# Kernel tuning notes

Measured on AMD Instinct MI355X. Metric: run time of the kernel, lower is better.

## Reference

```python
import jax, jax.numpy as jnp
import numpy as np

ALPHA = 0.9
EPS = 0.01
LAMBDA_PENALTY = 1.0
THRESHOLD = 0.8
COS_EPS = 1e-8
N, F, E = 8192, 256, 262144


def setup_inputs() -> dict:
    key = jax.random.key(0)
    k1, k2, k3, k4, k5 = jax.random.split(key, 5)
    z = jax.random.normal(k1, (N, F), dtype=jnp.float32)
    x_hat = jax.random.normal(k2, (N, F), dtype=jnp.float32)
    edge_index = jax.random.randint(k3, (2, E), 0, N, dtype=jnp.int64)
    f_k2u = jax.random.randint(k4, (N,), 0, 6, dtype=jnp.int64)
    f_u2k = jax.random.randint(k5, (N,), 0, 32, dtype=jnp.int64)
    return {"z": z, "x_hat": x_hat, "edge_index": edge_index,
            "f_k2u": f_k2u, "f_u2k": f_u2k, "epoch": 10}


def _corrcoef_features(z):
    # torch.corrcoef(z.T): correlation between the F feature columns over N nodes
    zm = z - jnp.mean(z, axis=0, keepdims=True)        # [N, F]
    cov = zm.T @ zm                                    # [F, F] (scale cancels in corr)
    std = jnp.sqrt(jnp.diag(cov))                      # [F]
    cor = cov / (std[:, None] * std[None, :])
    cor = jnp.clip(jnp.nan_to_num(cor), -1.0, 1.0)
    # fill_diagonal_(0)
    return cor * (1.0 - jnp.eye(cor.shape[0], dtype=cor.dtype))


def reference(z, x_hat, edge_index, f_k2u, f_u2k, epoch):
    n, f = z.shape
    zm = z - jnp.mean(z, axis=0, keepdims=True)
    cor = _corrcoef_features(z)                        # [F, F]
    # per-node scalar weight: alpha**f_k2u + (1 - alpha**f_u2k)
    w = (ALPHA ** f_k2u.astype(z.dtype)
         + (1.0 - ALPHA ** f_u2k.astype(z.dtype)))     # [N]
    W = w[:, None] * zm                                # [N, F]
    z2 = z + EPS * (W @ cor)                           # [N, F]

    # homophily (crash=True): per-edge cosine sim, scatter-add by source, degree-normalize
    i, j = edge_index[0], edge_index[1]
    zi, zj = z2[i], z2[j]                              # [E, F] gathers
    num = jnp.sum(zi * zj, axis=1)
    ni = jnp.maximum(jnp.linalg.norm(zi, axis=1), COS_EPS)
    nj = jnp.maximum(jnp.linalg.norm(zj, axis=1), COS_EPS)
    sim = num / (ni * nj)                              # [E]
    scores = jax.ops.segment_sum(sim, i, num_segments=n)
    deg = jax.ops.segment_sum(jnp.ones_like(sim), i, num_segments=n)
    deg = jnp.where(deg == 0, 1.0, deg)
    homophily_loss = -jnp.mean(scores / deg)

    # extra_loss (crash=True): dense NxN similarity masked by dense adjacency
    sim_mat = z2 @ z2.T                                # [N, N]
    adj = jnp.zeros((n, n), dtype=z.dtype)
    adj = adj.at[i, j].set(1.0).at[j, i].set(1.0)
    non_conn = sim_mat * (1.0 - adj)
    penalty = jnp.mean(jnp.where(non_conn > THRESHOLD, non_conn, 0.0))

    return homophily_loss + LAMBDA_PENALTY * penalty
```

## Files before the change

kernel.cpp:

```cpp
#include <hip/hip_runtime.h>
#include <stdint.h>
#include <math.h>

#define EPS_C 0.01f
#define THRESH 0.8f

constexpr int Nn = 8192;
constexpr int Ff = 256;
constexpr int Ee = 262144;

__device__ __forceinline__ float b2f(unsigned short u) {
  union { uint32_t i; float f; } v; v.i = ((uint32_t)u) << 16; return v.f;
}
__device__ __forceinline__ unsigned short f2b(float f) {
  union { uint32_t i; float f; } v; v.f = f;
  uint32_t r = v.i + 0x7FFFu + ((v.i >> 16) & 1u);
  return (unsigned short)(r >> 16);
}

typedef __bf16 bf16x8 __attribute__((ext_vector_type(8)));
typedef float f32x4 __attribute__((ext_vector_type(4)));
typedef int i32x4 __attribute__((ext_vector_type(4)));
typedef int i32x8 __attribute__((ext_vector_type(8)));

__global__ void k_transpose(const float* __restrict__ z, unsigned short* __restrict__ zT,
                            float* __restrict__ colsum) {
  __shared__ float Ls[64][65];
  int n0 = blockIdx.x * 64;
  int c0 = blockIdx.y * 64;
  int t = threadIdx.x;
  int r = t >> 4;
  int cq = t & 15;
#pragma unroll
  for (int i = 0; i < 4; ++i) {
    int row = r + 16 * i;
    float4 v = *(const float4*)(z + (size_t)(n0 + row) * Ff + c0 + cq * 4);
    Ls[row][cq * 4 + 0] = v.x;
    Ls[row][cq * 4 + 1] = v.y;
    Ls[row][cq * 4 + 2] = v.z;
    Ls[row][cq * 4 + 3] = v.w;
  }
  __syncthreads();
  if (t < 64) {
    float s = 0.f;
#pragma unroll
    for (int rr = 0; rr < 64; ++rr) s += Ls[rr][t];
    atomicAdd(&colsum[c0 + t], s);
  }
  int cr = t >> 4;
  int nq = t & 15;
#pragma unroll
  for (int i = 0; i < 4; ++i) {
    int c = cr + 16 * i;
    ushort4 o;
    o.x = f2b(Ls[nq * 4 + 0][c]);
    o.y = f2b(Ls[nq * 4 + 1][c]);
    o.z = f2b(Ls[nq * 4 + 2][c]);
    o.w = f2b(Ls[nq * 4 + 3][c]);
    *(ushort4*)(zT + (size_t)(c0 + c) * Nn + n0 + nq * 4) = o;
  }
}

__global__ __launch_bounds__(256, 2) void k_covg(const unsigned short* __restrict__ zT,
                                                 float* __restrict__ covp) {
  int bx = blockIdx.x, by = blockIdx.y, p = blockIdx.z;
  __shared__ __align__(16) unsigned short As[128 * 64];
  __shared__ __align__(16) unsigned short Bs[128 * 64];
  int t = threadIdx.x;
  int lane = t & 63, wv = t >> 6;
  int wr = wv >> 1, wc = wv & 1;
  int quad = lane >> 4, l15 = lane & 15;
  int a0 = by * 128, b0 = bx * 128;

  f32x4 acc[4][4];
#pragma unroll
  for (int i = 0; i < 4; ++i)
#pragma unroll
    for (int j = 0; j < 4; ++j) acc[i][j] = (f32x4){0.f, 0.f, 0.f, 0.f};

  for (int kk = 0; kk < 8; ++kk) {
    int k0 = p * 512 + kk * 64;
#pragma unroll
    for (int it = 0; it < 4; ++it) {
      int s = it * 256 + t;
      int r = s >> 3;
      int g = (s & 7) ^ (r & 7);
      const unsigned short* ga = zT + (size_t)(a0 + r) * Nn + k0 + g * 8;
      const unsigned short* gb = zT + (size_t)(b0 + r) * Nn + k0 + g * 8;
      __builtin_amdgcn_global_load_lds((const __attribute__((address_space(1))) void*)ga,
                                       (__attribute__((address_space(3))) void*)(As + s * 8),
                                       16, 0, 0);
      __builtin_amdgcn_global_load_lds((const __attribute__((address_space(1))) void*)gb,
                                       (__attribute__((address_space(3))) void*)(Bs + s * 8),
                                       16, 0, 0);
    }
    __syncthreads();
#pragma unroll
    for (int kc = 0; kc < 2; ++kc) {
      bf16x8 afr[4], bfr[4];
#pragma unroll
      for (int mt = 0; mt < 4; ++mt) {
        int rA = wr * 64 + mt * 16 + l15;
        int g = kc * 4 + quad;
        int gl = g ^ (rA & 7);
        afr[mt] = *(const bf16x8*)(As + ((size_t)rA * 8 + gl) * 8);
      }
#pragma unroll
      for (int nt = 0; nt < 4; ++nt) {
        int rB = wc * 64 + nt * 16 + l15;
        int g = kc * 4 + quad;
        int gl = g ^ (rB & 7);
        bfr[nt] = *(const bf16x8*)(Bs + ((size_t)rB * 8 + gl) * 8);
      }
#pragma unroll
      for (int mt = 0; mt < 4; ++mt)
#pragma unroll
        for (int nt = 0; nt < 4; ++nt)
          acc[mt][nt] = __builtin_amdgcn_mfma_f32_16x16x32_bf16(afr[mt], bfr[nt],
                                                                acc[mt][nt], 0, 0, 0);
    }
    __syncthreads();
  }

  float* outp = covp + (size_t)p * 65536;
#pragma unroll
  for (int mt = 0; mt < 4; ++mt)
#pragma unroll
    for (int r = 0; r < 4; ++r) {
      int a = a0 + wr * 64 + mt * 16 + quad * 4 + r;
#pragma unroll
      for (int nt = 0; nt < 4; ++nt) {
        int b = b0 + wc * 64 + nt * 16 + l15;
        outp[(size_t)a * Ff + b] = acc[mt][nt][r];
      }
    }
}

__global__ void k_cor(const float* __restrict__ covp, const float* __restrict__ colsum,
                      float* __restrict__ cor) {
  __shared__ float sd[256];
  int a = blockIdx.x, b = threadIdx.x;
  float mb = colsum[b] * (1.f / 8192.f);
  float gb = 0.f;
#pragma unroll
  for (int p = 0; p < 16; ++p) gb += covp[(size_t)p * 65536 + b * 257];
  float sb = sqrtf(gb - 8192.f * mb * mb);
  sd[b] = sb;
  float g = 0.f;
#pragma unroll
  for (int p = 0; p < 16; ++p) g += covp[(size_t)p * 65536 + a * Ff + b];
  __syncthreads();
  float c = 0.f;
  if (a != b) {
    float ma = colsum[a] * (1.f / 8192.f);
    float cv = g - 8192.f * ma * mb;
    c = cv / (sd[a] * sb);
    if (c != c) c = 0.f;
    c = fminf(1.f, fmaxf(-1.f, c));
  }
  cor[a * Ff + b] = c;
}

__global__ __launch_bounds__(256) void k_z2(const float* __restrict__ z,
    const float* __restrict__ colsum, const int* __restrict__ k2u,
    const int* __restrict__ u2k, const float* __restrict__ cor,
    unsigned short* __restrict__ z2b, unsigned char* __restrict__ z2f8,
    float* __restrict__ norms) {
  __shared__ float Wl[16 * 256];
  __shared__ float ws_[16];
  int t = threadIdx.x;
  int row0 = blockIdx.x * 16;
  if (t < 16) {
    int row = row0 + t;
    ws_[t] = powf(0.9f, (float)k2u[row]) + 1.f - powf(0.9f, (float)u2k[row]);
  }
  __syncthreads();
  float mt = colsum[t] * (1.f / 8192.f);
#pragma unroll
  for (int rr = 0; rr < 16; ++rr) {
    int row = row0 + rr;
    Wl[rr * 256 + t] = ws_[rr] * (z[(size_t)row * Ff + t] - mt);
  }
  __syncthreads();
  int tc = t & 63, tr = t >> 6;
  float acc[4][4];
#pragma unroll
  for (int i = 0; i < 4; ++i)
#pragma unroll
    for (int j = 0; j < 4; ++j) acc[i][j] = 0.f;
  const float* corc = cor + tc * 4;
  for (int k = 0; k < 256; ++k) {
    float4 c4 = *(const float4*)(corc + (size_t)k * 256);
#pragma unroll
    for (int rr = 0; rr < 4; ++rr) {
      float wv = Wl[(tr * 4 + rr) * 256 + k];
      acc[rr][0] = fmaf(wv, c4.x, acc[rr][0]);
      acc[rr][1] = fmaf(wv, c4.y, acc[rr][1]);
      acc[rr][2] = fmaf(wv, c4.z, acc[rr][2]);
      acc[rr][3] = fmaf(wv, c4.w, acc[rr][3]);
    }
  }
#pragma unroll
  for (int rr = 0; rr < 4; ++rr) {
    int row = row0 + tr * 4 + rr;
    float4 zv = *(const float4*)(z + (size_t)row * Ff + tc * 4);
    float x0 = zv.x + EPS_C * acc[rr][0];
    float x1 = zv.y + EPS_C * acc[rr][1];
    float x2 = zv.z + EPS_C * acc[rr][2];
    float x3 = zv.w + EPS_C * acc[rr][3];
    ushort4 o;
    o.x = f2b(x0); o.y = f2b(x1); o.z = f2b(x2); o.w = f2b(x3);
    *(ushort4*)(z2b + (size_t)row * Ff + tc * 4) = o;
    int pk = __builtin_amdgcn_cvt_pk_fp8_f32(x0, x1, 0, 0);
    pk = __builtin_amdgcn_cvt_pk_fp8_f32(x2, x3, pk, 1);
    *(unsigned int*)(z2f8 + (size_t)row * Ff + tc * 4) = (unsigned int)pk;
    float s = x0 * x0 + x1 * x1 + x2 * x2 + x3 * x3;
#pragma unroll
    for (int m = 1; m < 64; m <<= 1) s += __shfl_xor(s, m);
    if (tc == 0) norms[row] = fmaxf(sqrtf(s), 1e-8f);
  }
}

__global__ void k_adj(const int* __restrict__ ei, const int* __restrict__ ej,
                      unsigned int* __restrict__ adj) {
  int e = blockIdx.x * 256 + threadIdx.x;
  unsigned int i = (unsigned int)ei[e], j = (unsigned int)ej[e];
  size_t b1 = (size_t)i * Nn + j;
  size_t b2 = (size_t)j * Nn + i;
  atomicOr(&adj[b1 >> 5], 1u << (b1 & 31));
  atomicOr(&adj[b2 >> 5], 1u << (b2 & 31));
}

__global__ __launch_bounds__(256) void k_edge(const int* __restrict__ ei,
                       const int* __restrict__ ej,
                       const unsigned short* __restrict__ z2b,
                       const float* __restrict__ norms,
                       float* __restrict__ scores, float* __restrict__ deg) {
  int t = threadIdx.x;
  int wv = t >> 6, lane = t & 63;
  int half = lane >> 5;
  int l32 = lane & 31;
  int gw = blockIdx.x * 4 + wv;
  int ebase = gw * 32;
#pragma unroll 2
  for (int it = 0; it < 16; ++it) {
    int e = ebase + it * 2 + half;
    int i = ei[e], j = ej[e];
    uint4 ua = *(const uint4*)(z2b + (size_t)i * Ff + l32 * 8);
    uint4 ub = *(const uint4*)(z2b + (size_t)j * Ff + l32 * 8);
    float d = 0.f;
    const uint32_t* pa = (const uint32_t*)&ua;
    const uint32_t* pb = (const uint32_t*)&ub;
#pragma unroll
    for (int q = 0; q < 4; ++q) {
      union { uint32_t u; float f; } alo, ahi, blo, bhi;
      alo.u = pa[q] << 16;  ahi.u = pa[q] & 0xffff0000u;
      blo.u = pb[q] << 16;  bhi.u = pb[q] & 0xffff0000u;
      d = fmaf(alo.f, blo.f, d);
      d = fmaf(ahi.f, bhi.f, d);
    }
#pragma unroll
    for (int m = 1; m < 32; m <<= 1) d += __shfl_xor(d, m);
    if (l32 == 0) {
      float sim = d / (norms[i] * norms[j]);
      atomicAdd(&scores[i], sim);
      atomicAdd(&deg[i], 1.f);
    }
  }
}

__global__ __launch_bounds__(256, 2) void k_penalty(const unsigned char* __restrict__ z2f8,
    const unsigned int* __restrict__ adj, float* __restrict__ pp) {
  int tb = blockIdx.x;
  int br = (int)(64.5 - sqrt(64.5 * 64.5 - 2.0 * (double)tb));
  while ((br + 1) * 64 - ((br + 1) * br) / 2 <= tb) ++br;
  while (br * 64 - (br * (br - 1)) / 2 > tb) --br;
  int bc = br + (tb - (br * 64 - (br * (br - 1)) / 2));

  __shared__ __align__(16) unsigned char LB[65536];
  int t = threadIdx.x;
  int lane = t & 63;
  int wv = t >> 6;
  int wr = wv >> 1, wc = wv & 1;
  int quad = lane >> 4;
  int l15 = lane & 15;
  int arow0 = br * 128, brow0 = bc * 128;

  f32x4 acc[4][4];
#pragma unroll
  for (int i = 0; i < 4; ++i)
#pragma unroll
    for (int j = 0; j < 4; ++j) acc[i][j] = (f32x4){0.f, 0.f, 0.f, 0.f};

#define ISSUE_PHASE(p)                                                                   \
  {                                                                                      \
    unsigned char* buf = LB + (p) * 32768;                                               \
    int k0 = (p) * 128;                                                                  \
    _Pragma("unroll")                                                                    \
    for (int it = 0; it < 4; ++it) {                                                     \
      int s = it * 256 + t;                                                              \
      int r = s >> 3;                                                                    \
      int g = (s & 7) ^ (r & 7);                                                         \
      const unsigned char* ga = z2f8 + (size_t)(arow0 + r) * Ff + k0 + g * 16;           \
      const unsigned char* gb = z2f8 + (size_t)(brow0 + r) * Ff + k0 + g * 16;           \
      __builtin_amdgcn_global_load_lds((const __attribute__((address_space(1))) void*)ga,\
                                       (__attribute__((address_space(3))) void*)(buf + s * 16),      \
                                       16, 0, 0);                                        \
      __builtin_amdgcn_global_load_lds((const __attribute__((address_space(1))) void*)gb,\
                                       (__attribute__((address_space(3))) void*)(buf + 16384 + s * 16),\
                                       16, 0, 0);                                        \
    }                                                                                    \
  }

  ISSUE_PHASE(0)
  ISSUE_PHASE(1)
#pragma unroll
  for (int p = 0; p < 2; ++p) {
    if (p == 0) __builtin_amdgcn_s_waitcnt(0xF78);
    else        __builtin_amdgcn_s_waitcnt(0xF70);
    __builtin_amdgcn_s_barrier();
    const unsigned char* As = LB + p * 32768;
    const unsigned char* Bs = As + 16384;
    i32x8 a8[4], b8[4];
#pragma unroll
    for (int mt = 0; mt < 4; ++mt) {
      int rA = wr * 64 + mt * 16 + l15;
      int g0 = (2 * quad) ^ (rA & 7), g1 = (2 * quad + 1) ^ (rA & 7);
      i32x4 lo = *(const i32x4*)(As + rA * 128 + g0 * 16);
      i32x4 hi = *(const i32x4*)(As + rA * 128 + g1 * 16);
      a8[mt] = (i32x8){lo[0], lo[1], lo[2], lo[3], hi[0], hi[1], hi[2], hi[3]};
    }
#pragma unroll
    for (int nt = 0; nt < 4; ++nt) {
      int rB = wc * 64 + nt * 16 + l15;
      int g0 = (2 * quad) ^ (rB & 7), g1 = (2 * quad + 1) ^ (rB & 7);
      i32x4 lo = *(const i32x4*)(Bs + rB * 128 + g0 * 16);
      i32x4 hi = *(const i32x4*)(Bs + rB * 128 + g1 * 16);
      b8[nt] = (i32x8){lo[0], lo[1], lo[2], lo[3], hi[0], hi[1], hi[2], hi[3]};
    }
#pragma unroll
    for (int mt = 0; mt < 4; ++mt)
#pragma unroll
      for (int nt = 0; nt < 4; ++nt)
        acc[mt][nt] = __builtin_amdgcn_mfma_scale_f32_16x16x128_f8f6f4(
            a8[mt], b8[nt], acc[mt][nt], 0, 0,
            0, 0x7F7F7F7F, 0, 0x7F7F7F7F);
  }
#undef ISSUE_PHASE

  float local = 0.f;
  int a_base = arow0 + wr * 64;
  int b_base = brow0 + wc * 64;
#pragma unroll
  for (int mt = 0; mt < 4; ++mt) {
#pragma unroll
    for (int r = 0; r < 4; ++r) {
      int a = a_base + mt * 16 + quad * 4 + r;
      uint64_t bits = *(const uint64_t*)(adj + (size_t)a * 256 + (b_base >> 5));
#pragma unroll
      for (int nt = 0; nt < 4; ++nt) {
        float v = acc[mt][nt][r];
        int boff = nt * 16 + l15;
        bool conn = (bits >> boff) & 1ull;
        float wgt;
        if (br != bc) wgt = 2.f;
        else {
          int b = b_base + boff;
          wgt = (a < b) ? 2.f : (a == b ? 1.f : 0.f);
        }
        if (!conn && v > THRESH) local += wgt * v;
      }
    }
  }
#pragma unroll
  for (int m = 1; m < 64; m <<= 1) local += __shfl_xor(local, m);
  __syncthreads();
  float* red = (float*)LB;
  if (lane == 0) red[wv] = local;
  __syncthreads();
  if (t == 0) pp[tb] = red[0] + red[1] + red[2] + red[3];
}

__global__ void k_final(const float* __restrict__ scores, const float* __restrict__ deg,
                        const float* __restrict__ pp, float* __restrict__ out) {
  __shared__ float redh[4];
  __shared__ float redp[4];
  int t = threadIdx.x;
  float acch = 0.f;
#pragma unroll 4
  for (int it = 0; it < 32; ++it) {
    int n = it * 256 + t;
    float dg = deg[n];
    acch += scores[n] / (dg == 0.f ? 1.f : dg);
  }
  float accp = 0.f;
#pragma unroll
  for (int it = 0; it < 9; ++it) {
    int idx = it * 256 + t;
    if (idx < 2080) accp += pp[idx];
  }
#pragma unroll
  for (int m = 1; m < 64; m <<= 1) {
    acch += __shfl_xor(acch, m);
    accp += __shfl_xor(accp, m);
  }
  if ((t & 63) == 0) { redh[t >> 6] = acch; redp[t >> 6] = accp; }
  __syncthreads();
  if (t == 0) {
    double h = -(double)(redh[0] + redh[1] + redh[2] + redh[3]) / 8192.0;
    double p = (double)(redp[0] + redp[1] + redp[2] + redp[3]) / (8192.0 * 8192.0);
    out[0] = (float)(h + p);
  }
}

extern "C" void kernel_launch(void* const* d_in, const int* in_sizes, int n_in,
                              void* d_out, int out_size, void* d_ws, size_t ws_size,
                              hipStream_t stream) {
  const float* z = (const float*)d_in[0];
  const int* ei = (const int*)d_in[2];
  const int* ej = ei + Ee;
  const int* k2u = (const int*)d_in[3];
  const int* u2k = (const int*)d_in[4];

  char* ws = (char*)d_ws;
  unsigned int* adj = (unsigned int*)(ws);
  float* colsum     = (float*)(ws + 8388608);
  float* scores     = (float*)(ws + 8389632);
  float* deg        = (float*)(ws + 8422400);
  const size_t ZERO_BYTES = 8455168;
  float* covp       = (float*)(ws + 8455296);
  unsigned short* zT  = (unsigned short*)(ws + 12649600);
  unsigned short* z2b = (unsigned short*)(ws + 16843904);
  float* cor        = (float*)(ws + 21038208);
  float* norms      = (float*)(ws + 21300352);
  float* pp         = (float*)(ws + 21333120);
  unsigned char* z2f8 = (unsigned char*)(ws + 21341568);

  hipMemsetAsync(d_ws, 0, ZERO_BYTES, stream);
  k_adj<<<1024, 256, 0, stream>>>(ei, ej, adj);
  k_transpose<<<dim3(128, 4), 256, 0, stream>>>(z, zT, colsum);
  k_covg<<<dim3(2, 2, 16), 256, 0, stream>>>(zT, covp);
  k_cor<<<256, 256, 0, stream>>>(covp, colsum, cor);
  k_z2<<<512, 256, 0, stream>>>(z, colsum, k2u, u2k, cor, z2b, z2f8, norms);
  k_edge<<<2048, 256, 0, stream>>>(ei, ej, z2b, norms, scores, deg);
  k_penalty<<<2080, 256, 0, stream>>>(z2f8, adj, pp);
  k_final<<<1, 256, 0, stream>>>(scores, deg, pp, (float*)d_out);
}
```

Baseline: 205.1 us.

## Merge independent kernels horizontally to overlap adjacency build and edge scoring

The adjacency bitmap construction is folded into the covariance GEMM launch as extra blocks, and the per-edge cosine scoring is folded into the penalty GEMM launch as trailing blocks. This removes two kernel launches and lets latency-bound atomic and gather work overlap with the compute-heavy GEMM tiles on idle CUs. The trade-off is that the edge blocks now carry the penalty kernel's 64KB shared memory allocation and launch bounds, which may lower their occupancy.

```diff
diff --git a/kernel.cpp b/kernel.cpp
--- a/kernel.cpp
+++ b/kernel.cpp
@@ -61,12 +61,23 @@
   }
 }
 
-__global__ __launch_bounds__(256, 2) void k_covg(const unsigned short* __restrict__ zT,
-                                                 float* __restrict__ covp) {
-  int bx = blockIdx.x, by = blockIdx.y, p = blockIdx.z;
+__global__ __launch_bounds__(256, 2) void k_covg_adj(const unsigned short* __restrict__ zT,
+    float* __restrict__ covp, const int* __restrict__ ei, const int* __restrict__ ej,
+    unsigned int* __restrict__ adj) {
   __shared__ __align__(16) unsigned short As[128 * 64];
   __shared__ __align__(16) unsigned short Bs[128 * 64];
   int t = threadIdx.x;
+  if (blockIdx.x >= 64) {
+    int e = (blockIdx.x - 64) * 256 + t;
+    unsigned int i = (unsigned int)ei[e], j = (unsigned int)ej[e];
+    size_t b1 = (size_t)i * Nn + j;
+    size_t b2 = (size_t)j * Nn + i;
+    atomicOr(&adj[b1 >> 5], 1u << (b1 & 31));
+    atomicOr(&adj[b2 >> 5], 1u << (b2 & 31));
+    return;
+  }
+  int tb = blockIdx.x;
+  int bx = tb & 1, by = (tb >> 1) & 1, p = tb >> 2;
   int lane = t & 63, wv = t >> 6;
   int wr = wv >> 1, wc = wv & 1;
   int quad = lane >> 4, l15 = lane & 15;
@@ -221,66 +232,55 @@
   }
 }
 
-__global__ void k_adj(const int* __restrict__ ei, const int* __restrict__ ej,
-                      unsigned int* __restrict__ adj) {
-  int e = blockIdx.x * 256 + threadIdx.x;
-  unsigned int i = (unsigned int)ei[e], j = (unsigned int)ej[e];
-  size_t b1 = (size_t)i * Nn + j;
-  size_t b2 = (size_t)j * Nn + i;
-  atomicOr(&adj[b1 >> 5], 1u << (b1 & 31));
-  atomicOr(&adj[b2 >> 5], 1u << (b2 & 31));
-}
-
-__global__ __launch_bounds__(256) void k_edge(const int* __restrict__ ei,
-                       const int* __restrict__ ej,
-                       const unsigned short* __restrict__ z2b,
-                       const float* __restrict__ norms,
-                       float* __restrict__ scores, float* __restrict__ deg) {
+__global__ __launch_bounds__(256, 2) void k_edge_penalty(const unsigned char* __restrict__ z2f8,
+    const unsigned int* __restrict__ adj, float* __restrict__ pp,
+    const int* __restrict__ ei, const int* __restrict__ ej,
+    const unsigned short* __restrict__ z2b, const float* __restrict__ norms,
+    float* __restrict__ scores, float* __restrict__ deg) {
+  __shared__ __align__(16) unsigned char LB[65536];
   int t = threadIdx.x;
-  int wv = t >> 6, lane = t & 63;
-  int half = lane >> 5;
-  int l32 = lane & 31;
-  int gw = blockIdx.x * 4 + wv;
-  int ebase = gw * 32;
+  int lane = t & 63;
+  int wv = t >> 6;
+
+  if (blockIdx.x >= 2080) {
+    int half = lane >> 5;
+    int l32 = lane & 31;
+    int gw = (blockIdx.x - 2080) * 4 + wv;
+    int ebase = gw * 32;
 #pragma unroll 2
-  for (int it = 0; it < 16; ++it) {
-    int e = ebase + it * 2 + half;
-    int i = ei[e], j = ej[e];
-    uint4 ua = *(const uint4*)(z2b + (size_t)i * Ff + l32 * 8);
-    uint4 ub = *(const uint4*)(z2b + (size_t)j * Ff + l32 * 8);
-    float d = 0.f;
-    const uint32_t* pa = (const uint32_t*)&ua;
-    const uint32_t* pb = (const uint32_t*)&ub;
-#pragma unroll
-    for (int q = 0; q < 4; ++q) {
-      union { uint32_t u; float f; } alo, ahi, blo, bhi;
-      alo.u = pa[q] << 16;  ahi.u = pa[q] & 0xffff0000u;
-      blo.u = pb[q] << 16;  bhi.u = pb[q] & 0xffff0000u;
-      d = fmaf(alo.f, blo.f, d);
-      d = fmaf(ahi.f, bhi.f, d);
-    }
-#pragma unroll
-    for (int m = 1; m < 32; m <<= 1) d += __shfl_xor(d, m);
-    if (l32 == 0) {
-      float sim = d / (norms[i] * norms[j]);
-      atomicAdd(&scores[i], sim);
-      atomicAdd(&deg[i], 1.f);
-    }
-  }
-}
-
-__global__ __launch_bounds__(256, 2) void k_penalty(const unsigned char* __restrict__ z2f8,
-    const unsigned int* __restrict__ adj, float* __restrict__ pp) {
+    for (int it = 0; it < 16; ++it) {
+      int e = ebase + it * 2 + half;
+      int i = ei[e], j = ej[e];
+      uint4 ua = *(const uint4*)(z2b + (size_t)i * Ff + l32 * 8);
+      uint4 ub = *(const uint4*)(z2b + (size_t)j * Ff + l32 * 8);
+      float d = 0.f;
+      const uint32_t* pa = (const uint32_t*)&ua;
+      const uint32_t* pb = (const uint32_t*)&ub;
+#pragma unroll
+      for (int q = 0; q < 4; ++q) {
+        union { uint32_t u; float f; } alo, ahi, blo, bhi;
+        alo.u = pa[q] << 16;  ahi.u = pa[q] & 0xffff0000u;
+        blo.u = pb[q] << 16;  bhi.u = pb[q] & 0xffff0000u;
+        d = fmaf(alo.f, blo.f, d);
+        d = fmaf(ahi.f, bhi.f, d);
+      }
+#pragma unroll
+      for (int m = 1; m < 32; m <<= 1) d += __shfl_xor(d, m);
+      if (l32 == 0) {
+        float sim = d / (norms[i] * norms[j]);
+        atomicAdd(&scores[i], sim);
+        atomicAdd(&deg[i], 1.f);
+      }
+    }
+    return;
+  }
+
   int tb = blockIdx.x;
   int br = (int)(64.5 - sqrt(64.5 * 64.5 - 2.0 * (double)tb));
   while ((br + 1) * 64 - ((br + 1) * br) / 2 <= tb) ++br;
   while (br * 64 - (br * (br - 1)) / 2 > tb) --br;
   int bc = br + (tb - (br * 64 - (br * (br - 1)) / 2));
 
-  __shared__ __align__(16) unsigned char LB[65536];
-  int t = threadIdx.x;
-  int lane = t & 63;
-  int wv = t >> 6;
   int wr = wv >> 1, wc = wv & 1;
   int quad = lane >> 4;
   int l15 = lane & 15;
@@ -437,12 +437,10 @@
   unsigned char* z2f8 = (unsigned char*)(ws + 21341568);
 
   hipMemsetAsync(d_ws, 0, ZERO_BYTES, stream);
-  k_adj<<<1024, 256, 0, stream>>>(ei, ej, adj);
   k_transpose<<<dim3(128, 4), 256, 0, stream>>>(z, zT, colsum);
-  k_covg<<<dim3(2, 2, 16), 256, 0, stream>>>(zT, covp);
+  k_covg_adj<<<1088, 256, 0, stream>>>(zT, covp, ei, ej, adj);
   k_cor<<<256, 256, 0, stream>>>(covp, colsum, cor);
   k_z2<<<512, 256, 0, stream>>>(z, colsum, k2u, u2k, cor, z2b, z2f8, norms);
-  k_edge<<<2048, 256, 0, stream>>>(ei, ej, z2b, norms, scores, deg);
-  k_penalty<<<2080, 256, 0, stream>>>(z2f8, adj, pp);
+  k_edge_penalty<<<4128, 256, 0, stream>>>(z2f8, adj, pp, ei, ej, z2b, norms, scores, deg);
   k_final<<<1, 256, 0, stream>>>(scores, deg, pp, (float*)d_out);
 }
```

New measurement: 248.5 us. 1.21x slower.
